# Kernel optimization log

Hardware: AMD Instinct MI355X
Metric: run time of the kernel (lower is better)

The kernel has to match this reference:

```python
import jax, jax.numpy as jnp
import numpy as np

VOCAB = 32000
D = 128          # dim_model == dim_embed
H = 8            # heads
DK = D // H
DFF = 512
NL = 4           # layers
NCLS = 10
N = 131072       # total tree nodes
NLEAF = 65536
ERAND = 524288   # random tree edges; self-loops appended -> E = ERAND + N
NREAD = 4096
MAXPOS = 2048


def _pe_table():
    # standard sinusoidal positional encoding table [MAXPOS, D]
    p = jnp.arange(MAXPOS, dtype=jnp.float32)[:, None]
    div = jnp.exp(jnp.arange(0, D, 2, dtype=jnp.float32) * (-np.log(10000.0) / D))
    ang = p * div
    pe = jnp.zeros((MAXPOS, D), jnp.float32)
    pe = pe.at[:, 0::2].set(jnp.sin(ang)).at[:, 1::2].set(jnp.cos(ang))
    return pe


def _ln(x, g, b, eps=1e-5):
    m = jnp.mean(x, axis=-1, keepdims=True)
    v = jnp.mean(jnp.square(x - m), axis=-1, keepdims=True)
    return (x - m) * jax.lax.rsqrt(v + eps) * g + b


def setup_inputs() -> dict:
    key = jax.random.key(0)
    ks = jax.random.split(key, 32)
    s = 1.0 / np.sqrt(D)
    inp = {}
    # graph / token inputs
    inp['x'] = jax.random.randint(ks[0], (NLEAF,), 0, VOCAB)
    inp['pos'] = jax.random.randint(ks[1], (NLEAF,), 0, MAXPOS)
    inp['leaf_ids'] = jnp.arange(NLEAF)
    src = jax.random.randint(ks[2], (ERAND,), 0, N)
    dst = jax.random.randint(ks[3], (ERAND,), 0, N)
    loops = jnp.arange(N)  # self loops so every node has >=1 incoming edge
    inp['src'] = jnp.concatenate([src, loops])
    inp['dst'] = jnp.concatenate([dst, loops])
    inp['readout_ids'] = jax.random.randint(ks[4], (NREAD,), 0, N)
    inp['h0'] = jnp.zeros((N, D), jnp.float32)  # internal nodes start at zero
    # parameters
    inp['embed_table'] = jax.random.normal(ks[5], (VOCAB, D)) * 0.02
    inp['emb_ng'] = jnp.ones((D,)); inp['emb_nb'] = jnp.zeros((D,))
    inp['Wq'] = jax.random.normal(ks[6], (NL, D, D)) * s
    inp['bq'] = jnp.zeros((NL, D))
    inp['Wk'] = jax.random.normal(ks[7], (NL, D, D)) * s
    inp['bk'] = jnp.zeros((NL, D))
    inp['Wv'] = jax.random.normal(ks[8], (NL, D, D)) * s
    inp['bv'] = jnp.zeros((NL, D))
    inp['Wo'] = jax.random.normal(ks[9], (NL, D, D)) * s
    inp['bo'] = jnp.zeros((NL, D))
    inp['ln1_g'] = jnp.ones((NL, D)); inp['ln1_b'] = jnp.zeros((NL, D))
    inp['W1'] = jax.random.normal(ks[10], (NL, D, DFF)) * s
    inp['b1'] = jnp.zeros((NL, DFF))
    inp['W2'] = jax.random.normal(ks[11], (NL, DFF, D)) * (1.0 / np.sqrt(DFF))
    inp['b2'] = jnp.zeros((NL, D))
    inp['ln2_g'] = jnp.ones((NL, D)); inp['ln2_b'] = jnp.zeros((NL, D))
    inp['gen_W'] = jax.random.normal(ks[12], (D, NCLS)) * s
    inp['gen_b'] = jnp.zeros((NCLS,))
    return inp


def reference(embed_table, emb_ng, emb_nb, Wq, bq, Wk, bk, Wv, bv, Wo, bo,
              ln1_g, ln1_b, W1, b1, W2, b2, ln2_g, ln2_b, gen_W, gen_b,
              h0, x, pos, leaf_ids, src, dst, readout_ids):
    pe = _pe_table()
    # leaf embedding (scaled, since rel_pos=False) + positional encoding, then LayerNorm
    hl = embed_table[x] * jnp.sqrt(jnp.float32(D)) + pe[pos]
    hl = _ln(hl, emb_ng, emb_nb)
    h = h0.at[leaf_ids].set(hl)  # [N, D]
    inv = 1.0 / np.sqrt(DK)
    for i in range(NL):
        q = (h @ Wq[i] + bq[i]).reshape(N, H, DK)
        k = (h @ Wk[i] + bk[i]).reshape(N, H, DK)
        v = (h @ Wv[i] + bv[i]).reshape(N, H, DK)
        # per-edge scaled dot-product scores [E, H]
        score = jnp.einsum('ehd,ehd->eh', q[dst], k[src]) * inv
        m = jax.lax.stop_gradient(jax.ops.segment_max(score, dst, num_segments=N))
        ex = jnp.exp(score - m[dst])
        den = jax.ops.segment_sum(ex, dst, num_segments=N)  # [N, H]
        agg = jax.ops.segment_sum(ex[:, :, None] * v[src], dst, num_segments=N)
        agg = agg / den[:, :, None]  # [N, H, DK]
        o = agg.reshape(N, D) @ Wo[i] + bo[i]
        h = _ln(h + o, ln1_g[i], ln1_b[i])
        ff = jax.nn.relu(h @ W1[i] + b1[i]) @ W2[i] + b2[i]
        h = _ln(h + ff, ln2_g[i], ln2_b[i])
    hr = h[readout_ids]
    return jax.nn.log_softmax(hr @ gen_W + gen_b, axis=-1)
```

## Files before the change

kernel.cpp:

```cpp
#include <hip/hip_runtime.h>
#include <hip/hip_bf16.h>

#define D 128
#define DFF 512
#define NLAYER 4
#define NCLS 10
#define NN 131072
#define NLEAF 65536
#define ETOT 655360
#define NREAD 4096

typedef unsigned short u16;
typedef unsigned int u32;
typedef __attribute__((ext_vector_type(8))) short bf16x8;
typedef __attribute__((ext_vector_type(16))) float f32x16;

#define MFMA32(a,b,c) __builtin_amdgcn_mfma_f32_32x32x16_bf16(a,b,c,0,0,0)

__device__ __forceinline__ float b2f(u16 u){ u32 x = ((u32)u)<<16; return __builtin_bit_cast(float, x); }
__device__ __forceinline__ u16 f2b(float f){ u32 i = __builtin_bit_cast(u32, f); u32 r = (i + 0x7FFFu + ((i>>16)&1u))>>16; return (u16)r; }
__device__ __forceinline__ float blo(u32 u){ return __builtin_bit_cast(float, u<<16); }
__device__ __forceinline__ float bhi(u32 u){ return __builtin_bit_cast(float, u & 0xffff0000u); }

__device__ __forceinline__ float wredsum(float v){
  v += __shfl_xor(v,32); v += __shfl_xor(v,16); v += __shfl_xor(v,8);
  v += __shfl_xor(v,4);  v += __shfl_xor(v,2);  v += __shfl_xor(v,1);
  return v;
}
__device__ __forceinline__ float rsum32(float v){
  v += __shfl_xor(v,1); v += __shfl_xor(v,2); v += __shfl_xor(v,4);
  v += __shfl_xor(v,8); v += __shfl_xor(v,16);
  return v;
}

__device__ __forceinline__ bf16x8 ldfrag(const u16* buf, int row, int kbyte){
  return *(const bf16x8*)((const char*)buf + row*256 + ((u32)kbyte ^ (u32)((row&7)<<4)));
}

__device__ __forceinline__ void stage_B(const u16* __restrict__ src, int strideElems, int colOff,
                                        u16* BsBase, int wv_, int lane){
  int rb = wv_*32 + (lane>>4);
  int slotbase = lane & 15;
  #pragma unroll
  for(int it=0; it<8; it++){
    int r = rb + it*4;
    int slot = slotbase ^ (r&7);
    __builtin_amdgcn_global_load_lds(
      (const __attribute__((address_space(1))) unsigned*)(src + (size_t)r*strideElems + colOff + slot*8),
      (__attribute__((address_space(3))) unsigned*)((char*)BsBase + wv_*8192 + it*1024),
      16, 0, 0);
  }
}

__device__ __forceinline__ void mfma_regA(const bf16x8 af[8], const u16* Bs,
                                          int l31, int lkh, f32x16 acc[4]){
  #pragma unroll
  for(int kk=0;kk<8;kk++){
    #pragma unroll
    for(int c=0;c<4;c++){
      bf16x8 bf = ldfrag(Bs, c*32 + l31, kk*32 + lkh);
      acc[c] = MFMA32(af[kk], bf, acc[c]);
    }
  }
}

__device__ __forceinline__ void ln_epilogue(f32x16 acc[4], size_t r0, int wrow0, int l31, int h5,
    const float* g, const float* b, u16* hb){
  float gc[4], bc[4];
  #pragma unroll
  for(int c=0;c<4;c++){ int col = c*32 + l31; gc[c]=g[col]; bc[c]=b[col]; }
  #pragma unroll
  for(int r=0;r<16;r++){
    int rowl = wrow0 + (r&3) + 8*(r>>2) + 4*h5;
    size_t base = (r0 + rowl)*(size_t)D;
    float v[4];
    #pragma unroll
    for(int c=0;c<4;c++) v[c] = acc[c][r] + b2f(hb[base + c*32 + l31]);
    float s = rsum32(v[0]+v[1]+v[2]+v[3]);
    float mean = s * (1.0f/128.0f);
    float dd[4]; float q = 0.f;
    #pragma unroll
    for(int c=0;c<4;c++){ dd[c]=v[c]-mean; q += dd[c]*dd[c]; }
    q = rsum32(q);
    float rs = rsqrtf(q*(1.0f/128.0f) + 1e-5f);
    #pragma unroll
    for(int c=0;c<4;c++){
      float o = dd[c]*rs*gc[c] + bc[c];
      hb[base + c*32 + l31] = f2b(o);
    }
  }
}

__global__ __launch_bounds__(256) void k_hinit(const float* __restrict__ h0, u16* __restrict__ hb){
  int i = blockIdx.x*256 + threadIdx.x;
  float4 v = ((const float4*)h0)[i];
  ushort4 p; p.x=f2b(v.x); p.y=f2b(v.y); p.z=f2b(v.z); p.w=f2b(v.w);
  ((ushort4*)hb)[i] = p;
}

__global__ __launch_bounds__(256) void k_embed(const int* __restrict__ x, const int* __restrict__ pos,
    const int* __restrict__ leaf, const float* __restrict__ emb,
    const float* __restrict__ g, const float* __restrict__ b, u16* __restrict__ hb){
  int row = blockIdx.x*4 + (threadIdx.x>>6);
  int lane = threadIdx.x & 63;
  int tok = x[row]; float p = (float)pos[row];
  float v[2];
  #pragma unroll
  for(int j=0;j<2;j++){
    int d = lane + 64*j;
    float freq = expf(-0.07195578515529633f * (float)(d & ~1));
    float ang = p * freq;
    float pe = (d&1) ? cosf(ang) : sinf(ang);
    v[j] = emb[(size_t)tok*D + d] * 11.313708498984761f + pe;
  }
  float mean = wredsum(v[0]+v[1]) * (1.0f/128.0f);
  float d0 = v[0]-mean, d1 = v[1]-mean;
  float var = wredsum(d0*d0 + d1*d1) * (1.0f/128.0f);
  float rs = rsqrtf(var + 1e-5f);
  size_t orow = (size_t)leaf[row];
  hb[orow*D + lane]      = f2b(d0*rs*g[lane]    + b[lane]);
  hb[orow*D + lane + 64] = f2b(d1*rs*g[lane+64] + b[lane+64]);
}

__global__ __launch_bounds__(256) void k_wconv(const float* __restrict__ Wq, const float* __restrict__ Wk,
    const float* __restrict__ Wv, const float* __restrict__ Wo,
    const float* __restrict__ W1, const float* __restrict__ W2,
    u16* __restrict__ wqt, u16* __restrict__ wkt, u16* __restrict__ wvt, u16* __restrict__ wot,
    u16* __restrict__ w1t, u16* __restrict__ w2t){
  int e = blockIdx.x*256 + threadIdx.x;
  int l = e / 196608, r = e % 196608;
  if(r < 65536){
    int w = r >> 14, i = r & 16383;
    int n = i >> 7, k = i & 127;
    const float* src = (w==0)?Wq:(w==1)?Wk:(w==2)?Wv:Wo;
    u16* dst = (w==0)?wqt:(w==1)?wkt:(w==2)?wvt:wot;
    dst[l*16384 + n*128 + k] = f2b(src[l*16384 + k*128 + n]);
  } else if(r < 131072){
    int i = r - 65536; int n = i >> 7, k = i & 127;
    w1t[l*65536 + n*128 + k] = f2b(W1[l*65536 + k*512 + n]);
  } else {
    int i = r - 131072; int n = i >> 9, f = i & 511;
    w2t[l*65536 + n*512 + f] = f2b(W2[l*65536 + f*128 + n]);
  }
}

__global__ __launch_bounds__(256) void k_count(const int* __restrict__ dst, int* __restrict__ cnt){
  int e = blockIdx.x*256 + threadIdx.x;
  atomicAdd(&cnt[dst[e]], 1);
}
__global__ __launch_bounds__(256) void k_scan1(const int* __restrict__ cnt, int* __restrict__ part,
                                               int* __restrict__ bsum){
  __shared__ int s[256];
  int tid = threadIdx.x; int i = blockIdx.x*256 + tid;
  int v = cnt[i]; s[tid]=v; __syncthreads();
  for(int off=1; off<256; off<<=1){
    int t=(tid>=off)? s[tid-off]:0; __syncthreads();
    s[tid]+=t; __syncthreads();
  }
  part[i] = s[tid]-v;
  if(tid==255) bsum[blockIdx.x] = s[255];
}
__global__ __launch_bounds__(512) void k_scan2(int* __restrict__ bsum){
  __shared__ int s[512];
  int tid = threadIdx.x;
  int v = bsum[tid]; s[tid] = v; __syncthreads();
  for(int off=1; off<512; off<<=1){
    int t = (tid>=off)? s[tid-off]:0; __syncthreads();
    s[tid] += t; __syncthreads();
  }
  bsum[tid] = s[tid] - v;
}
__global__ __launch_bounds__(256) void k_scan3(const int* __restrict__ part, const int* __restrict__ bsum,
                                               int* __restrict__ indptr, int* __restrict__ cursor){
  int i = blockIdx.x*256 + threadIdx.x;
  int v = part[i] + bsum[i>>8];
  indptr[i] = v; cursor[i] = v;
  if(i==0) indptr[NN] = ETOT;
}
__global__ __launch_bounds__(256) void k_scatter(const int* __restrict__ src, const int* __restrict__ dst,
    int* __restrict__ cursor, int* __restrict__ esrc){
  int e = blockIdx.x*256 + threadIdx.x;
  int p = atomicAdd(&cursor[dst[e]], 1);
  esrc[p] = src[e];
}

__global__ __launch_bounds__(256,2) void k_qkv(const u16* __restrict__ hb,
    const u16* __restrict__ wqt, const u16* __restrict__ wkt, const u16* __restrict__ wvt,
    const float* __restrict__ bq, const float* __restrict__ bk, const float* __restrict__ bv,
    u16* __restrict__ qb, u16* __restrict__ kb, u16* __restrict__ vb){
  __shared__ u16 Bs[128*128];
  int tid = threadIdx.x;
  int lane = tid & 63, wv_ = tid >> 6;
  int l31 = lane & 31, h5 = lane >> 5, lkh = h5*16;
  int wrow0 = wv_*32;
  size_t r0 = (size_t)blockIdx.x * 128;
  int widx = blockIdx.y;
  const u16* wt = (widx==0)?wqt:(widx==1)?wkt:wvt;
  const float* bias = (widx==0)?bq:(widx==1)?bk:bv;
  u16* op = (widx==0)?qb:(widx==1)?kb:vb;

  stage_B(wt, D, 0, Bs, wv_, lane);
  bf16x8 af[8];
  const u16* arow = hb + (r0 + wrow0 + l31)*(size_t)D + h5*8;
  #pragma unroll
  for(int kk=0;kk<8;kk++) af[kk] = *(const bf16x8*)(arow + kk*16);

  f32x16 acc[4];
  #pragma unroll
  for(int c=0;c<4;c++){
    float bb = bias[c*32+l31];
    #pragma unroll
    for(int i=0;i<16;i++) acc[c][i] = bb;
  }
  __syncthreads();
  mfma_regA(af, Bs, l31, lkh, acc);
  #pragma unroll
  for(int c=0;c<4;c++){
    int col = c*32 + l31;
    #pragma unroll
    for(int r=0;r<16;r++){
      int row = wrow0 + (r&3) + 8*(r>>2) + 4*h5;
      op[(r0+row)*(size_t)D + col] = f2b(acc[c][r]);
    }
  }
}

__global__ __launch_bounds__(256,6) void k_attn(const u16* qb, const u16* __restrict__ kb,
    const u16* __restrict__ vb, const int* __restrict__ indptr, const int* __restrict__ esrc,
    u16* aggb){
  int node = blockIdx.x*4 + (threadIdx.x>>6);
  int lane = threadIdx.x & 63;
  int hd = lane >> 3, eslot = lane & 7;
  int beg = indptr[node], end = indptr[node+1];
  float qr[16];
  {
    const uint4* qp = (const uint4*)(qb + (size_t)node*D + hd*16);
    uint4 a = qp[0], b = qp[1];
    u32 w[8] = {a.x,a.y,a.z,a.w,b.x,b.y,b.z,b.w};
    #pragma unroll
    for(int i=0;i<8;i++){ qr[2*i] = blo(w[i])*0.25f; qr[2*i+1] = bhi(w[i])*0.25f; }
  }
  float m = -3.0e38f, den = 0.f;
  float acc[16];
  #pragma unroll
  for(int i=0;i<16;i++) acc[i] = 0.f;
  for(int e0=beg; e0<end; e0+=8){
    int e = e0 + eslot;
    if(e < end){
      int s = esrc[e];
      const uint4* kp = (const uint4*)(kb + (size_t)s*D + hd*16);
      uint4 k0 = kp[0], k1 = kp[1];
      const uint4* vp = (const uint4*)(vb + (size_t)s*D + hd*16);
      uint4 v0 = vp[0], v1 = vp[1];
      u32 kw[8] = {k0.x,k0.y,k0.z,k0.w,k1.x,k1.y,k1.z,k1.w};
      float p = 0.f, p2 = 0.f;
      #pragma unroll
      for(int i=0;i<8;i++){ p = fmaf(blo(kw[i]), qr[2*i], p); p2 = fmaf(bhi(kw[i]), qr[2*i+1], p2); }
      p += p2;
      float nm = fmaxf(m, p);
      float fs = __expf(m - nm);
      float w  = __expf(p - nm);
      den = den*fs + w;
      u32 vw[8] = {v0.x,v0.y,v0.z,v0.w,v1.x,v1.y,v1.z,v1.w};
      #pragma unroll
      for(int i=0;i<8;i++){
        acc[2*i]   = fmaf(acc[2*i],   fs, w*blo(vw[i]));
        acc[2*i+1] = fmaf(acc[2*i+1], fs, w*bhi(vw[i]));
      }
      m = nm;
    }
  }
  float mo = m;
  #pragma unroll
  for(int s=1; s<8; s<<=1){
    float m2 = __shfl_xor(m, s); float d2 = __shfl_xor(den, s);
    float nm = fmaxf(m, m2);
    den = den*__expf(m-nm) + d2*__expf(m2-nm);
    m = nm;
  }
  float scale = __expf(mo - m) / den;
  #pragma unroll
  for(int i=0;i<16;i++) acc[i] *= scale;
  #pragma unroll
  for(int s=1; s<8; s<<=1){
    #pragma unroll
    for(int i=0;i<16;i++) acc[i] += __shfl_xor(acc[i], s);
  }
  if(eslot == 0){
    u32 pk[8];
    #pragma unroll
    for(int i=0;i<8;i++) pk[i] = (u32)f2b(acc[2*i]) | ((u32)f2b(acc[2*i+1])<<16);
    uint4* dp = (uint4*)(aggb + (size_t)node*D + hd*16);
    dp[0] = make_uint4(pk[0],pk[1],pk[2],pk[3]);
    dp[1] = make_uint4(pk[4],pk[5],pk[6],pk[7]);
  }
}

__global__ __launch_bounds__(256,2) void k_owo(const u16* __restrict__ aggb, const u16* __restrict__ wot,
    const float* __restrict__ bo, const float* __restrict__ g1, const float* __restrict__ b1,
    u16* hb){
  __shared__ u16 Bs[128*128];
  int tid = threadIdx.x;
  int lane = tid & 63, wv_ = tid >> 6;
  int l31 = lane & 31, h5 = lane >> 5, lkh = h5*16;
  int wrow0 = wv_*32;
  size_t r0 = (size_t)blockIdx.x * 128;
  stage_B(wot, D, 0, Bs, wv_, lane);
  bf16x8 af[8];
  const u16* arow = aggb + (r0 + wrow0 + l31)*(size_t)D + h5*8;
  #pragma unroll
  for(int kk=0;kk<8;kk++) af[kk] = *(const bf16x8*)(arow + kk*16);
  f32x16 acc[4];
  #pragma unroll
  for(int c=0;c<4;c++){
    float bb = bo[c*32+l31];
    #pragma unroll
    for(int i=0;i<16;i++) acc[c][i] = bb;
  }
  __syncthreads();
  mfma_regA(af, Bs, l31, lkh, acc);
  ln_epilogue(acc, r0, wrow0, l31, h5, g1, b1, hb);
}

__global__ __launch_bounds__(256,2) void k_ffn(const u16* __restrict__ w1t, const u16* __restrict__ w2t,
    const float* __restrict__ b1, const float* __restrict__ b2,
    const float* __restrict__ g2, const float* __restrict__ bb2,
    u16* hb){
  __shared__ u16 Bs[128*128];
  __shared__ u16 Ts[128*128];
  int tid = threadIdx.x;
  int lane = tid & 63, wv_ = tid >> 6;
  int l31 = lane & 31, h5 = lane >> 5, lkh = h5*16;
  int wrow0 = wv_*32;
  size_t r0 = (size_t)blockIdx.x * 128;
  bf16x8 af[8];
  const u16* arow = hb + (r0 + wrow0 + l31)*(size_t)D + h5*8;
  #pragma unroll
  for(int kk=0;kk<8;kk++) af[kk] = *(const bf16x8*)(arow + kk*16);
  f32x16 out[4];
  #pragma unroll
  for(int c=0;c<4;c++){
    float bb = b2[c*32+l31];
    #pragma unroll
    for(int i=0;i<16;i++) out[c][i] = bb;
  }
  for(int ch=0; ch<4; ch++){
    if(ch) __syncthreads();
    stage_B(w1t + ch*128*D, D, 0, Bs, wv_, lane);
    __syncthreads();
    f32x16 tacc[4];
    #pragma unroll
    for(int c=0;c<4;c++){
      float bb = b1[ch*128 + c*32 + l31];
      #pragma unroll
      for(int i=0;i<16;i++) tacc[c][i] = bb;
    }
    mfma_regA(af, Bs, l31, lkh, tacc);
    #pragma unroll
    for(int c=0;c<4;c++){
      int tcol = c*32 + l31;
      #pragma unroll
      for(int r=0;r<16;r++){
        int trow = wrow0 + (r&3) + 8*(r>>2) + 4*h5;
        *(u16*)((char*)Ts + trow*256 + (u32)((tcol*2) ^ ((trow&7)<<4))) = f2b(fmaxf(tacc[c][r],0.f));
      }
    }
    __syncthreads();
    stage_B(w2t, DFF, ch*128, Bs, wv_, lane);
    __syncthreads();
    bf16x8 taf[8];
    #pragma unroll
    for(int kk=0;kk<8;kk++) taf[kk] = ldfrag(Ts, wrow0 + l31, kk*32 + lkh);
    mfma_regA(taf, Bs, l31, lkh, out);
  }
  ln_epilogue(out, r0, wrow0, l31, h5, g2, bb2, hb);
}

__global__ __launch_bounds__(64) void k_readout(const u16* __restrict__ hb, const int* __restrict__ rid,
    const float* __restrict__ gw, const float* __restrict__ gb, float* __restrict__ out){
  int r = blockIdx.x; int lane = threadIdx.x;
  size_t node = (size_t)rid[r];
  float h0v = b2f(hb[node*D + lane]), h1v = b2f(hb[node*D + 64 + lane]);
  float lg[NCLS];
  #pragma unroll
  for(int c=0;c<NCLS;c++){
    float p = h0v*gw[lane*NCLS + c] + h1v*gw[(lane+64)*NCLS + c];
    lg[c] = wredsum(p) + gb[c];
  }
  float mx = lg[0];
  #pragma unroll
  for(int c=1;c<NCLS;c++) mx = fmaxf(mx, lg[c]);
  float se = 0.f;
  #pragma unroll
  for(int c=0;c<NCLS;c++) se += expf(lg[c]-mx);
  float lse = mx + logf(se);
  if(lane < NCLS) out[(size_t)r*NCLS + lane] = lg[lane] - lse;
}

extern "C" void kernel_launch(void* const* d_in, const int* in_sizes, int n_in,
                              void* d_out, int out_size, void* d_ws, size_t ws_size,
                              hipStream_t stream) {
  const int* x    = (const int*)d_in[0];
  const int* pos  = (const int*)d_in[1];
  const int* leaf = (const int*)d_in[2];
  const int* src  = (const int*)d_in[3];
  const int* dst  = (const int*)d_in[4];
  const int* rid  = (const int*)d_in[5];
  const float* h0 = (const float*)d_in[6];
  const float* emb= (const float*)d_in[7];
  const float* eng= (const float*)d_in[8];
  const float* enb= (const float*)d_in[9];
  const float* Wq = (const float*)d_in[10];
  const float* bq = (const float*)d_in[11];
  const float* Wk = (const float*)d_in[12];
  const float* bk = (const float*)d_in[13];
  const float* Wv = (const float*)d_in[14];
  const float* bv = (const float*)d_in[15];
  const float* Wo = (const float*)d_in[16];
  const float* bo = (const float*)d_in[17];
  const float* l1g= (const float*)d_in[18];
  const float* l1b= (const float*)d_in[19];
  const float* W1 = (const float*)d_in[20];
  const float* b1 = (const float*)d_in[21];
  const float* W2 = (const float*)d_in[22];
  const float* b2 = (const float*)d_in[23];
  const float* l2g= (const float*)d_in[24];
  const float* l2b= (const float*)d_in[25];
  const float* gw = (const float*)d_in[26];
  const float* gb = (const float*)d_in[27];
  float* out = (float*)d_out;

  char* ws = (char*)d_ws;
  u16* hb     = (u16*)(ws);
  u16* qb     = (u16*)(ws + 33554432);
  u16* kb     = (u16*)(ws + 67108864);
  u16* vb     = (u16*)(ws + 100663296);
  u16* wqt    = (u16*)(ws + 134217728);
  u16* wkt    = (u16*)(ws + 134348800);
  u16* wvt    = (u16*)(ws + 134479872);
  u16* wot    = (u16*)(ws + 134610944);
  u16* w1t    = (u16*)(ws + 134742016);
  u16* w2t    = (u16*)(ws + 135266304);
  int* indptr = (int*)(ws + 135790592);
  int* cursor = (int*)(ws + 136315136);
  int* part   = (int*)(ws + 136839424);
  int* bsum   = (int*)(ws + 137363712);
  int* esrc   = (int*)(ws + 137365760);

  k_hinit<<<NN*D/4/256, 256, 0, stream>>>(h0, hb);
  k_embed<<<NLEAF/4, 256, 0, stream>>>(x, pos, leaf, emb, eng, enb, hb);
  k_wconv<<<NLAYER*196608/256, 256, 0, stream>>>(Wq,Wk,Wv,Wo,W1,W2, wqt,wkt,wvt,wot,w1t,w2t);

  hipMemsetAsync(cursor, 0, NN*sizeof(int), stream);
  k_count  <<<ETOT/256, 256, 0, stream>>>(dst, cursor);
  k_scan1  <<<NN/256, 256, 0, stream>>>(cursor, part, bsum);
  k_scan2  <<<1, 512, 0, stream>>>(bsum);
  k_scan3  <<<NN/256, 256, 0, stream>>>(part, bsum, indptr, cursor);
  k_scatter<<<ETOT/256, 256, 0, stream>>>(src, dst, cursor, esrc);

  for(int l=0; l<NLAYER; l++){
    k_qkv<<<dim3(NN/128,3), 256, 0, stream>>>(hb, wqt + l*16384, wkt + l*16384, wvt + l*16384,
                                              bq + l*D, bk + l*D, bv + l*D, qb, kb, vb);
    k_attn<<<NN/4, 256, 0, stream>>>(qb, kb, vb, indptr, esrc, qb);
    k_owo<<<NN/128, 256, 0, stream>>>(qb, wot + l*16384, bo + l*D,
                                      l1g + l*D, l1b + l*D, hb);
    k_ffn<<<NN/128, 256, 0, stream>>>(w1t + l*65536, w2t + l*65536,
                                      b1 + l*DFF, b2 + l*D, l2g + l*D, l2b + l*D, hb);
  }
  k_readout<<<NREAD, 64, 0, stream>>>(hb, rid, gw, gb, out);
}
```

Measured before the change: 969.7 us.

## Keep FFN hidden activations in registers and rework attention reduction

The FFN kernel now computes the first GEMM transposed (weights as A operand), so the ReLU output can be repacked into A-operand fragments in registers through a cross-half-wave shuffle. This removes the LDS round trip for the hidden tile and one pair of barriers per chunk, and both weight chunks are staged together into two LDS buffers. The attention kernel replaces its full butterfly all-reduce of 16 accumulators with a recursive-halving reduce-scatter, so each lane writes one packed pair. It also raises occupancy bounds to 8 and moves the score scaling after the dot product. The risks are higher register pressure and correctness of the fragment-layout shuffles.

Result: no change. 975.9 us (+0.6%).

```diff
diff --git a/kernel.cpp b/kernel.cpp
--- a/kernel.cpp
+++ b/kernel.cpp
@@ -14,6 +14,7 @@
 typedef unsigned int u32;
 typedef __attribute__((ext_vector_type(8))) short bf16x8;
 typedef __attribute__((ext_vector_type(16))) float f32x16;
+typedef u32 u32x4 __attribute__((ext_vector_type(4)));
 
 #define MFMA32(a,b,c) __builtin_amdgcn_mfma_f32_32x32x16_bf16(a,b,c,0,0,0)
 
@@ -225,7 +226,7 @@
   }
 }
 
-__global__ __launch_bounds__(256,6) void k_attn(const u16* qb, const u16* __restrict__ kb,
+__global__ __launch_bounds__(256,8) void k_attn(const u16* qb, const u16* __restrict__ kb,
     const u16* __restrict__ vb, const int* __restrict__ indptr, const int* __restrict__ esrc,
     u16* aggb){
   int node = blockIdx.x*4 + (threadIdx.x>>6);
@@ -238,7 +239,7 @@
     uint4 a = qp[0], b = qp[1];
     u32 w[8] = {a.x,a.y,a.z,a.w,b.x,b.y,b.z,b.w};
     #pragma unroll
-    for(int i=0;i<8;i++){ qr[2*i] = blo(w[i])*0.25f; qr[2*i+1] = bhi(w[i])*0.25f; }
+    for(int i=0;i<8;i++){ qr[2*i] = blo(w[i]); qr[2*i+1] = bhi(w[i]); }
   }
   float m = -3.0e38f, den = 0.f;
   float acc[16];
@@ -256,7 +257,7 @@
       float p = 0.f, p2 = 0.f;
       #pragma unroll
       for(int i=0;i<8;i++){ p = fmaf(blo(kw[i]), qr[2*i], p); p2 = fmaf(bhi(kw[i]), qr[2*i+1], p2); }
-      p += p2;
+      p = (p + p2)*0.25f;
       float nm = fmaxf(m, p);
       float fs = __expf(m - nm);
       float w  = __expf(p - nm);
@@ -278,22 +279,27 @@
     den = den*__expf(m-nm) + d2*__expf(m2-nm);
     m = nm;
   }
-  float scale = __expf(mo - m) / den;
-  #pragma unroll
-  for(int i=0;i<16;i++) acc[i] *= scale;
-  #pragma unroll
-  for(int s=1; s<8; s<<=1){
-    #pragma unroll
-    for(int i=0;i<16;i++) acc[i] += __shfl_xor(acc[i], s);
-  }
-  if(eslot == 0){
-    u32 pk[8];
-    #pragma unroll
-    for(int i=0;i<8;i++) pk[i] = (u32)f2b(acc[2*i]) | ((u32)f2b(acc[2*i+1])<<16);
-    uint4* dp = (uint4*)(aggb + (size_t)node*D + hd*16);
-    dp[0] = make_uint4(pk[0],pk[1],pk[2],pk[3]);
-    dp[1] = make_uint4(pk[4],pk[5],pk[6],pk[7]);
-  }
+  float sc = __expf(mo - m);
+  #pragma unroll
+  for(int i=0;i<16;i++) acc[i] *= sc;
+  #pragma unroll
+  for(int lvl=0; lvl<3; lvl++){
+    const int half = 8 >> lvl;
+    const int msk = 1 << lvl;
+    bool hi = (eslot >> lvl) & 1;
+    #pragma unroll
+    for(int i=0;i<half;i++){
+      float a = acc[i], b = acc[i+half];
+      acc[i]      = hi ? b : a;
+      acc[i+half] = hi ? a : b;
+    }
+    #pragma unroll
+    for(int i=0;i<half;i++) acc[i] += __shfl_xor(acc[i+half], msk);
+  }
+  int base = (eslot&1)*8 + ((eslot>>1)&1)*4 + ((eslot>>2)&1)*2;
+  float rin = 1.0f/den;
+  u32 pk = (u32)f2b(acc[0]*rin) | ((u32)f2b(acc[1]*rin)<<16);
+  *(u32*)(aggb + (size_t)node*D + hd*16 + base) = pk;
 }
 
 __global__ __launch_bounds__(256,2) void k_owo(const u16* __restrict__ aggb, const u16* __restrict__ wot,
@@ -326,8 +332,8 @@
     const float* __restrict__ b1, const float* __restrict__ b2,
     const float* __restrict__ g2, const float* __restrict__ bb2,
     u16* hb){
-  __shared__ u16 Bs[128*128];
-  __shared__ u16 Ts[128*128];
+  __shared__ u16 B1s[128*128];
+  __shared__ u16 B2s[128*128];
   int tid = threadIdx.x;
   int lane = tid & 63, wv_ = tid >> 6;
   int l31 = lane & 31, h5 = lane >> 5, lkh = h5*16;
@@ -346,32 +352,60 @@
   }
   for(int ch=0; ch<4; ch++){
     if(ch) __syncthreads();
-    stage_B(w1t + ch*128*D, D, 0, Bs, wv_, lane);
+    stage_B(w1t + ch*128*D, D, 0, B1s, wv_, lane);
+    stage_B(w2t, DFF, ch*128, B2s, wv_, lane);
     __syncthreads();
-    f32x16 tacc[4];
+    f32x16 acc2[4];
     #pragma unroll
     for(int c=0;c<4;c++){
-      float bb = b1[ch*128 + c*32 + l31];
-      #pragma unroll
-      for(int i=0;i<16;i++) tacc[c][i] = bb;
-    }
-    mfma_regA(af, Bs, l31, lkh, tacc);
-    #pragma unroll
-    for(int c=0;c<4;c++){
-      int tcol = c*32 + l31;
       #pragma unroll
       for(int r=0;r<16;r++){
-        int trow = wrow0 + (r&3) + 8*(r>>2) + 4*h5;
-        *(u16*)((char*)Ts + trow*256 + (u32)((tcol*2) ^ ((trow&7)<<4))) = f2b(fmaxf(tacc[c][r],0.f));
+        int foff = (r&3) + 8*(r>>2) + 4*h5;
+        acc2[c][r] = b1[ch*128 + c*32 + foff];
       }
     }
-    __syncthreads();
-    stage_B(w2t, DFF, ch*128, Bs, wv_, lane);
-    __syncthreads();
-    bf16x8 taf[8];
-    #pragma unroll
-    for(int kk=0;kk<8;kk++) taf[kk] = ldfrag(Ts, wrow0 + l31, kk*32 + lkh);
-    mfma_regA(taf, Bs, l31, lkh, out);
+    #pragma unroll
+    for(int kk=0;kk<8;kk++){
+      #pragma unroll
+      for(int c=0;c<4;c++){
+        bf16x8 w1f = ldfrag(B1s, c*32 + l31, kk*32 + lkh);
+        acc2[c] = MFMA32(w1f, af[kk], acc2[c]);
+      }
+    }
+    bf16x8 af2[8];
+    bool hb5 = (h5 != 0);
+    #pragma unroll
+    for(int c=0;c<4;c++){
+      u32 pk[8];
+      #pragma unroll
+      for(int t=0;t<8;t++){
+        float lo  = fmaxf(acc2[c][2*t],   0.f);
+        float hi2 = fmaxf(acc2[c][2*t+1], 0.f);
+        u32 r_;
+        asm("v_cvt_pk_bf16_f32 %0, %1, %2" : "=v"(r_) : "v"(lo), "v"(hi2));
+        pk[t] = r_;
+      }
+      u32 s0 = hb5 ? pk[0] : pk[2];
+      u32 s1 = hb5 ? pk[1] : pk[3];
+      u32 s2 = hb5 ? pk[4] : pk[6];
+      u32 s3 = hb5 ? pk[5] : pk[7];
+      u32 g0 = (u32)__shfl_xor((int)s0, 32);
+      u32 g1 = (u32)__shfl_xor((int)s1, 32);
+      u32 g2_ = (u32)__shfl_xor((int)s2, 32);
+      u32 g3 = (u32)__shfl_xor((int)s3, 32);
+      u32x4 A0 = { hb5 ? g0 : pk[0], hb5 ? g1 : pk[1], hb5 ? pk[2] : g0, hb5 ? pk[3] : g1 };
+      u32x4 A1 = { hb5 ? g2_ : pk[4], hb5 ? g3 : pk[5], hb5 ? pk[6] : g2_, hb5 ? pk[7] : g3 };
+      af2[2*c]   = __builtin_bit_cast(bf16x8, A0);
+      af2[2*c+1] = __builtin_bit_cast(bf16x8, A1);
+    }
+    #pragma unroll
+    for(int kk=0;kk<8;kk++){
+      #pragma unroll
+      for(int c=0;c<4;c++){
+        bf16x8 w2f = ldfrag(B2s, c*32 + l31, kk*32 + lkh);
+        out[c] = MFMA32(af2[kk], w2f, out[c]);
+      }
+    }
   }
   ln_epilogue(out, r0, wrow0, l31, h5, g2, bb2, hb);
 }
```
